# Optimization experiments

Measured on AMD Instinct MI355X. Metric: run time of the kernel, lower is better.

The kernel has to match this reference:

```python
import jax, jax.numpy as jnp
from jax import lax
import numpy as np

NS, NC = 12, 4            # n_state, n_ctrl
NSC = NS + NC             # tau = [x; u]
T, B = 50, 2048
U_LO, U_HI = -1.0, 1.0
LQR_ITERS = 3             # qp_iter-style outer LQR iterations
N_LS = 5                  # max_linesearch_iter
LS_DECAY = 0.5            # linesearch_decay


def setup_inputs() -> dict:
    key = jax.random.key(0)
    k0, k1, k2, k3, k4 = jax.random.split(key, 5)
    x0 = jax.random.normal(k0, (B, NS), jnp.float32)
    # PD quadratic cost: C = 0.1 * A A^T + I  (symmetric positive definite)
    A = jax.random.normal(k1, (T, B, NSC, NSC), jnp.float32) * (1.0 / np.sqrt(NSC))
    C = 0.1 * jnp.einsum('tbik,tbjk->tbij', A, A) + jnp.eye(NSC, dtype=jnp.float32)
    c = jax.random.normal(k2, (T, B, NSC), jnp.float32)
    # Near-identity stable linear dynamics x' = F [x;u] + f
    F = 0.02 * jax.random.normal(k3, (T, B, NS, NSC), jnp.float32)
    eye_pad = jnp.concatenate([0.98 * jnp.eye(NS, dtype=jnp.float32),
                               jnp.zeros((NS, NC), jnp.float32)], axis=-1)
    F = F + eye_pad
    f = 0.01 * jax.random.normal(k4, (T, B, NS), jnp.float32)
    return {'x0': x0, 'C': C, 'c': c, 'F': F, 'f': f}


def _riccati(C, c, F, f):
    """Backward Riccati recursion. Returns feedback gains K [T,B,NC,NS], k [T,B,NC]."""
    def step(carry, inp):
        V, v = carry                      # V: [B,NS,NS], v: [B,NS]
        Ct, ct, Ft, ft = inp
        FtV = jnp.einsum('bki,bkl->bil', Ft, V)          # F^T V: [B,NSC,NS]
        Q = Ct + jnp.einsum('bil,blj->bij', FtV, Ft)     # [B,NSC,NSC]
        q = ct + jnp.einsum('bki,bk->bi', Ft,
                            jnp.einsum('bij,bj->bi', V, ft) + v)
        Qxx, Qxu = Q[:, :NS, :NS], Q[:, :NS, NS:]
        Qux, Quu = Q[:, NS:, :NS], Q[:, NS:, NS:]
        qx, qu = q[:, :NS], q[:, NS:]
        rhs = jnp.concatenate([Qux, qu[:, :, None]], axis=-1)  # [B,NC,NS+1]
        sol = jnp.linalg.solve(Quu, rhs)
        K = -sol[:, :, :NS]               # [B,NC,NS]
        kk = -sol[:, :, NS]               # [B,NC]
        QxuK = jnp.einsum('bij,bjk->bik', Qxu, K)
        V_new = Qxx + QxuK + QxuK.transpose(0, 2, 1) \
            + jnp.einsum('bji,bjl,blk->bik', K, Quu, K)
        V_new = 0.5 * (V_new + V_new.transpose(0, 2, 1))
        v_new = qx + jnp.einsum('bij,bj->bi', Qxu, kk) \
            + jnp.einsum('bji,bj->bi', K, qu + jnp.einsum('bij,bj->bi', Quu, kk))
        return (V_new, v_new), (K, kk)

    Vz = jnp.zeros((C.shape[1], NS, NS), C.dtype)
    vz = jnp.zeros((C.shape[1], NS), C.dtype)
    _, (K, kk) = lax.scan(step, (Vz, vz), (C, c, F, f), reverse=True)
    return K, kk


def _rollout(alpha, x0, u_nom, K, kk, C, c, F, f):
    """Forward pass with box-clamped controls and line-search blending."""
    def step(carry, inp):
        x, cost = carry
        Ct, ct, Ft, ft, Kt, kt, unomt = inp
        u_lqr = jnp.einsum('bij,bj->bi', Kt, x) + kt
        u = jnp.clip((1.0 - alpha) * unomt + alpha * u_lqr, U_LO, U_HI)
        tau = jnp.concatenate([x, u], axis=-1)            # [B,NSC]
        cost = cost + 0.5 * jnp.einsum('bi,bij,bj->b', tau, Ct, tau) \
            + jnp.einsum('bi,bi->b', ct, tau)
        x_next = jnp.einsum('bij,bj->bi', Ft, tau) + ft
        return (x_next, cost), tau

    init = (x0, jnp.zeros(x0.shape[0], x0.dtype))
    (_, cost), taus = lax.scan(step, init, (C, c, F, f, K, kk, u_nom))
    return cost, taus  # cost [B], taus [T,B,NSC]


def reference(x0, C, c, F, f):
    alphas = LS_DECAY ** jnp.arange(N_LS, dtype=C.dtype)  # [N_LS]
    u_nom = jnp.zeros((T, x0.shape[0], NC), x0.dtype)
    taus = None
    for _ in range(LQR_ITERS):
        K, kk = _riccati(C, c, F, f)
        costs, taus_all = jax.vmap(
            lambda a: _rollout(a, x0, u_nom, K, kk, C, c, F, f))(alphas)
        # costs: [N_LS,B]; taus_all: [N_LS,T,B,NSC]. Pick best alpha per batch elem.
        best = jnp.argmin(costs, axis=0)                  # [B]
        taus = jnp.take_along_axis(taus_all,
                                   best[None, None, :, None], axis=0)[0]
        u_nom = taus[:, :, NS:]
    return taus  # [T, B, NSC] optimized trajectory [x; u]
```

## Files before the change

### kernel.cpp

```cpp
#include <hip/hip_runtime.h>
#include <math.h>

#define T_   50
#define B_   2048
#define NS_  12
#define NC_  4
#define NSC_ 16
#define LDC  20
#define TAUS_STRIDE 808

__device__ __forceinline__ float dot4f(const float4 a, const float4 b) {
    return a.x*b.x + a.y*b.y + a.z*b.z + a.w*b.w;
}
__device__ __forceinline__ void axpy4(float4& acc, float s, const float4 v) {
    acc.x += s*v.x; acc.y += s*v.y; acc.z += s*v.z; acc.w += s*v.w;
}

__device__ __forceinline__ void wsync() {
    __builtin_amdgcn_wave_barrier();
    __builtin_amdgcn_s_waitcnt(0xC07F);
    __builtin_amdgcn_wave_barrier();
}

__device__ __forceinline__ void bsync() {
    asm volatile("s_waitcnt lgkmcnt(0)\n\ts_barrier" ::: "memory");
}

struct RicPref { float4 rC, rAux; };

__device__ __forceinline__ RicPref ric_load(
    const float* Cg, const float* cg, const float* Fg, const float* fg,
    int t, int b, int lane)
{
    RicPref p;
    const size_t base = (size_t)t * B_ + b;
    p.rC = ((const float4*)(Cg + base*256))[lane];
    if (lane < 48)      p.rAux = ((const float4*)(Fg + base*192))[lane];
    else if (lane < 52) p.rAux = ((const float4*)(cg + base*16))[lane-48];
    else if (lane < 55) p.rAux = ((const float4*)(fg + base*12))[lane-52];
    return p;
}

__global__ __launch_bounds__(64) void riccati_kernel(
    const float* __restrict__ Cg, const float* __restrict__ cg,
    const float* __restrict__ Fg, const float* __restrict__ fg,
    float* __restrict__ Kk)
{
    const int b    = blockIdx.x;
    const int lane = threadIdx.x;

    __shared__ __align__(16) float sV[144];
    __shared__ __align__(16) float sv[12];
    __shared__ __align__(16) float sF[12*LDC];
    __shared__ __align__(16) float sC[16*LDC];
    __shared__ __align__(16) float sc[16];
    __shared__ __align__(16) float sf[12];
    __shared__ __align__(16) float sP[12*LDC];
    __shared__ __align__(16) float sQ[16*LDC];
    __shared__ __align__(16) float sq[16];
    __shared__ __align__(16) float stmp[12];
    __shared__ __align__(16) float sK[48];
    __shared__ __align__(16) float skk[4];
    __shared__ __align__(16) float sM[144];

    for (int i = lane; i < 144; i += 64) sV[i] = 0.f;
    if (lane < 12) sv[lane] = 0.f;

    RicPref cur = ric_load(Cg, cg, Fg, fg, T_-1, b, lane);
    wsync();

    for (int t = T_ - 1; t >= 0; --t) {
        const size_t base = (size_t)t * B_ + b;

        wsync();
        {
            const int row = lane >> 2, ch = (lane & 3) << 2;
            *(float4*)(sC + row*LDC + ch) = cur.rC;
            if (lane < 48)      *(float4*)(sF + row*LDC + ch) = cur.rAux;
            else if (lane < 52) ((float4*)sc)[lane-48] = cur.rAux;
            else if (lane < 55) ((float4*)sf)[lane-52] = cur.rAux;
        }
        RicPref nxt = ric_load(Cg, cg, Fg, fg, (t > 0) ? t-1 : 0, b, lane);
        wsync();

        if (lane < 48) {
            const int k = lane >> 2, jc = (lane & 3) << 2;
            float4 acc = make_float4(0.f,0.f,0.f,0.f);
            #pragma unroll
            for (int l = 0; l < 12; ++l) {
                axpy4(acc, sV[k*12 + l], *(const float4*)(sF + l*LDC + jc));
            }
            *(float4*)(sP + k*LDC + jc) = acc;
        } else if (lane < 60) {
            const int k = lane - 48;
            float acc = sv[k];
            #pragma unroll
            for (int l = 0; l < 12; ++l) acc += sV[k*12 + l] * sf[l];
            stmp[k] = acc;
        }
        wsync();

        {
            const int i = lane >> 2, jc = (lane & 3) << 2;
            float4 acc = *(const float4*)(sC + i*LDC + jc);
            #pragma unroll
            for (int k = 0; k < 12; ++k) {
                axpy4(acc, sF[k*LDC + i], *(const float4*)(sP + k*LDC + jc));
            }
            *(float4*)(sQ + i*LDC + jc) = acc;
        }
        if (lane < 16) {
            float acc = sc[lane];
            #pragma unroll
            for (int k = 0; k < 12; ++k) acc += sF[k*LDC + lane] * stmp[k];
            sq[lane] = acc;
        }
        wsync();

        {
            const float* Qu = sQ + 12*LDC + 12;
            const float a00=Qu[0],      a01=Qu[1],      a02=Qu[2],      a03=Qu[3];
            const float a11=Qu[LDC+1],  a12=Qu[LDC+2],  a13=Qu[LDC+3];
            const float a22=Qu[2*LDC+2],a23=Qu[2*LDC+3],a33=Qu[3*LDC+3];
            const float l00 = sqrtf(a00), i00 = 1.f/l00;
            const float l10 = a01*i00, l20 = a02*i00, l30 = a03*i00;
            const float l11 = sqrtf(a11 - l10*l10), i11 = 1.f/l11;
            const float l21 = (a12 - l20*l10)*i11;
            const float l31 = (a13 - l30*l10)*i11;
            const float l22 = sqrtf(a22 - l20*l20 - l21*l21), i22 = 1.f/l22;
            const float l32 = (a23 - l30*l20 - l31*l21)*i22;
            const float l33 = sqrtf(a33 - l30*l30 - l31*l31 - l32*l32), i33 = 1.f/l33;
            if (lane < 13) {
                float r0, r1, r2, r3;
                if (lane < 12) {
                    r0 = sQ[12*LDC + lane]; r1 = sQ[13*LDC + lane];
                    r2 = sQ[14*LDC + lane]; r3 = sQ[15*LDC + lane];
                } else {
                    r0 = sq[12]; r1 = sq[13]; r2 = sq[14]; r3 = sq[15];
                }
                const float y0 = r0*i00;
                const float y1 = (r1 - l10*y0)*i11;
                const float y2 = (r2 - l20*y0 - l21*y1)*i22;
                const float y3 = (r3 - l30*y0 - l31*y1 - l32*y2)*i33;
                const float z3 = y3*i33;
                const float z2 = (y2 - l32*z3)*i22;
                const float z1 = (y1 - l21*z2 - l31*z3)*i11;
                const float z0 = (y0 - l10*z1 - l20*z2 - l30*z3)*i00;
                if (lane < 12) {
                    sK[0*12+lane] = -z0; sK[1*12+lane] = -z1;
                    sK[2*12+lane] = -z2; sK[3*12+lane] = -z3;
                } else {
                    skk[0] = -z0; skk[1] = -z1; skk[2] = -z2; skk[3] = -z3;
                }
            }
        }
        wsync();

        if (lane < 52) {
            (Kk + base*52)[lane] = (lane < 48) ? sK[lane] : skk[lane-48];
        }
        if (lane < 36) {
            const int i = lane / 3, jc = (lane % 3) << 2;
            float4 acc = make_float4(0.f,0.f,0.f,0.f);
            #pragma unroll
            for (int m = 0; m < 4; ++m) {
                axpy4(acc, sK[m*12 + i], *(const float4*)(sQ + (12+m)*LDC + jc));
            }
            *(float4*)(sM + i*12 + jc) = acc;
        } else if (lane < 48) {
            const int i = lane - 36;
            float acc = sq[i];
            #pragma unroll
            for (int m = 0; m < 4; ++m) acc += sQ[i*LDC + 12 + m] * skk[m];
            sv[i] = acc;
        }
        wsync();

        if (lane < 36) {
            const int i = lane / 3, jc = (lane % 3) << 2;
            const float4 q  = *(const float4*)(sQ + i*LDC + jc);
            const float4 m1 = *(const float4*)(sM + i*12 + jc);
            const float t0 = sM[(jc+0)*12 + i];
            const float t1 = sM[(jc+1)*12 + i];
            const float t2 = sM[(jc+2)*12 + i];
            const float t3 = sM[(jc+3)*12 + i];
            float4 r;
            r.x = q.x + 0.5f*(m1.x + t0);
            r.y = q.y + 0.5f*(m1.y + t1);
            r.z = q.z + 0.5f*(m1.z + t2);
            r.w = q.w + 0.5f*(m1.w + t3);
            *(float4*)(sV + i*12 + jc) = r;
        }
        cur = nxt;
    }
}

struct RollAux { float4 r1, r2; };

__device__ __forceinline__ RollAux aux_load(
    const float* cg, const float* Fg, const float* fg, const float* Kk,
    int t, int b, int lane)
{
    RollAux p;
    const size_t base = (size_t)t * B_ + b;
    if (lane < 48)      p.r1 = ((const float4*)(Fg + base*192))[lane];
    else if (lane < 61) p.r1 = ((const float4*)(Kk + base*52))[lane-48];
    else                p.r1 = ((const float4*)(cg + base*16))[lane-61];
    if (lane == 0)      p.r2 = ((const float4*)(cg + base*16))[3];
    else if (lane < 4)  p.r2 = ((const float4*)(fg + base*12))[lane-1];
    return p;
}

__global__ __launch_bounds__(128, 4) void rollout_kernel(
    const float* __restrict__ x0g, const float* __restrict__ Cg,
    const float* __restrict__ cg,  const float* __restrict__ Fg,
    const float* __restrict__ fg,  const float* __restrict__ Kk,
    float* __restrict__ outg)
{
    const int b    = blockIdx.x;
    const int tid  = threadIdx.x;
    const int wave = tid >> 6;
    const int lane = tid & 63;

    __shared__ __align__(16) float staus[5*TAUS_STRIDE];
    __shared__ __align__(16) float sunom[T_*NC_];
    __shared__ __align__(16) float sx0[12];
    __shared__ __align__(16) float sC[16*LDC];
    __shared__ __align__(16) float sF[12*LDC];
    __shared__ __align__(16) float sKk[56];
    __shared__ __align__(16) float sc[16];
    __shared__ __align__(16) float sf[12];
    __shared__ float scost[5];
    __shared__ int   sbest;

    const int  task    = wave*64 + lane;
    const bool is_cost = task < 80;
    int a1, i1;
    if (is_cost) { a1 = task >> 4; i1 = task & 15; }
    else { const int v = task - 80; a1 = v / 12; i1 = v - a1*12; }
    const float* row1  = (is_cost ? (const float*)sC : (const float*)sF) + i1*LDC;
    const float* add1  = (is_cost ? (const float*)sc : (const float*)sf) + i1;
    float*       taub1 = staus + a1*TAUS_STRIDE;

    const int    iT    = (lane < 12) ? lane : 0;
    const float* rowT  = sF + iT*LDC;
    float*       taubT = staus + 4*TAUS_STRIDE;

    const int    aA  = (lane < 20) ? (lane >> 2) : 0;
    const int    iA  = lane & 3;
    const float  alA = ldexpf(1.0f, -aA);
    const float* KrA = sKk + iA*12;
    float*       tauA = staus + aA*TAUS_STRIDE;

    for (int i = tid; i < T_*NC_; i += 128) sunom[i] = 0.f;
    if (tid < 3) ((float4*)sx0)[tid] = ((const float4*)(x0g + (size_t)b*12))[tid];

    float4  curC;
    RollAux curA;
    if (wave == 0) curC = ((const float4*)(Cg + (size_t)b*256))[lane];
    else           curA = aux_load(cg, Fg, fg, Kk, 0, b, lane);
    bsync();

    for (int iter = 0; iter < 3; ++iter) {
        if (tid < 15) {
            const int a = tid / 3, ch = (tid % 3) << 2;
            *(float4*)(staus + a*TAUS_STRIDE + ch) = *(const float4*)(sx0 + ch);
        }
        float ca = 0.f;
        int toff = 0;

        for (int t = 0; t < T_; ++t) {
            bsync();
            if (wave == 0) {
                const int row = lane >> 2, ch = (lane & 3) << 2;
                *(float4*)(sC + row*LDC + ch) = curC;
                curC = ((const float4*)(Cg +
                          ((size_t)((t+1 < T_) ? t+1 : 0) * B_ + b)*256))[lane];
            } else {
                {
                    const int row = lane >> 2, ch = (lane & 3) << 2;
                    if (lane < 48)      *(float4*)(sF + row*LDC + ch) = curA.r1;
                    else if (lane < 61) ((float4*)sKk)[lane-48] = curA.r1;
                    else                ((float4*)sc)[lane-61]  = curA.r1;
                    if (lane == 0)      ((float4*)sc)[3] = curA.r2;
                    else if (lane < 4)  ((float4*)sf)[lane-1] = curA.r2;
                }
                curA = aux_load(cg, Fg, fg, Kk, (t+1 < T_) ? t+1 : 0, b, lane);
                wsync();
                if (lane < 20) {
                    const float* x = tauA + toff;
                    float ulqr = dot4f(*(const float4*)(KrA+0), *(const float4*)(x+0))
                               + dot4f(*(const float4*)(KrA+4), *(const float4*)(x+4))
                               + dot4f(*(const float4*)(KrA+8), *(const float4*)(x+8))
                               + sKk[48 + iA];
                    float u = (1.f - alA)*sunom[t*4 + iA] + alA*ulqr;
                    u = fminf(1.f, fmaxf(-1.f, u));
                    tauA[toff + 12 + iA] = u;
                }
            }
            bsync();

            const bool tnl = (t != T_-1);
            {
                const float* tau = taub1 + toff;
                const float  av  = add1[0];
                float acc = is_cost ? 0.f : av;
                acc += dot4f(*(const float4*)(row1+ 0), *(const float4*)(tau+ 0));
                acc += dot4f(*(const float4*)(row1+ 4), *(const float4*)(tau+ 4));
                acc += dot4f(*(const float4*)(row1+ 8), *(const float4*)(tau+ 8));
                acc += dot4f(*(const float4*)(row1+12), *(const float4*)(tau+12));
                if (is_cost)  ca += (0.5f*acc + av) * tau[i1];
                else if (tnl) taub1[toff + 16 + i1] = acc;
            }
            if (wave == 0 && lane < 12 && tnl) {
                const float* tau = taubT + toff;
                float acc = sf[iT];
                acc += dot4f(*(const float4*)(rowT+ 0), *(const float4*)(tau+ 0));
                acc += dot4f(*(const float4*)(rowT+ 4), *(const float4*)(tau+ 4));
                acc += dot4f(*(const float4*)(rowT+ 8), *(const float4*)(tau+ 8));
                acc += dot4f(*(const float4*)(rowT+12), *(const float4*)(tau+12));
                taubT[toff + 16 + iT] = acc;
            }
            toff += 16;
        }

        #pragma unroll
        for (int off = 1; off < 16; off <<= 1) ca += __shfl_xor(ca, off, 16);
        if (wave == 0) { if ((lane & 15) == 0) scost[lane >> 4] = ca; }
        else if (lane == 0) scost[4] = ca;
        bsync();
        if (tid == 0) {
            int bi = 0; float bc = scost[0];
            #pragma unroll
            for (int a = 1; a < 5; ++a) {
                if (scost[a] < bc) { bc = scost[a]; bi = a; }
            }
            sbest = bi;
        }
        bsync();
        const int best = sbest;

        for (int idx = tid; idx < T_*NC_; idx += 128) {
            const int tt = idx >> 2, i = idx & 3;
            sunom[idx] = staus[best*TAUS_STRIDE + tt*16 + 12 + i];
        }
        if (iter == 2) {
            for (int idx = tid; idx < T_*NSC_; idx += 128) {
                const int tt = idx >> 4, j = idx & 15;
                outg[((size_t)tt*B_ + b)*16 + j] = staus[best*TAUS_STRIDE + tt*16 + j];
            }
        }
        bsync();
    }
}

extern "C" void kernel_launch(void* const* d_in, const int* in_sizes, int n_in,
                              void* d_out, int out_size, void* d_ws, size_t ws_size,
                              hipStream_t stream) {
    const float* x0 = (const float*)d_in[0];
    const float* C  = (const float*)d_in[1];
    const float* c  = (const float*)d_in[2];
    const float* F  = (const float*)d_in[3];
    const float* f  = (const float*)d_in[4];
    float* out = (float*)d_out;
    float* Kk  = (float*)d_ws;

    riccati_kernel<<<B_, 64, 0, stream>>>(C, c, F, f, Kk);
    rollout_kernel<<<B_, 128, 0, stream>>>(x0, C, c, F, f, Kk, out);
}
```

Measured before the change: 444.2 us.

## Prefetch per-thread cost/dynamics rows into registers, drop shared staging

Each thread now loads from global memory, into registers, exactly the C/F row, the c/f scalar and the K row it needs for the next timestep, double-buffered across unrolled steps. This removes the shared-memory staging of C, F, K, c and f along with the extra wave sync. It also splits the dot products around the block barrier so the x-part is computed before u is known. The cost is more registers per thread and redundant or uncoalesced global loads, and occupancy could suffer under the launch bounds.

```diff
diff --git a/kernel.cpp b/kernel.cpp
--- a/kernel.cpp
+++ b/kernel.cpp
@@ -195,21 +195,7 @@
     }
 }
 
-struct RollAux { float4 r1, r2; };
-
-__device__ __forceinline__ RollAux aux_load(
-    const float* cg, const float* Fg, const float* fg, const float* Kk,
-    int t, int b, int lane)
-{
-    RollAux p;
-    const size_t base = (size_t)t * B_ + b;
-    if (lane < 48)      p.r1 = ((const float4*)(Fg + base*192))[lane];
-    else if (lane < 61) p.r1 = ((const float4*)(Kk + base*52))[lane-48];
-    else                p.r1 = ((const float4*)(cg + base*16))[lane-61];
-    if (lane == 0)      p.r2 = ((const float4*)(cg + base*16))[3];
-    else if (lane < 4)  p.r2 = ((const float4*)(fg + base*12))[lane-1];
-    return p;
-}
+struct RollPref { float4 row[4]; float4 aux[4]; float s0, s1; };
 
 __global__ __launch_bounds__(128, 4) void rollout_kernel(
     const float* __restrict__ x0g, const float* __restrict__ Cg,
@@ -225,11 +211,6 @@
     __shared__ __align__(16) float staus[5*TAUS_STRIDE];
     __shared__ __align__(16) float sunom[T_*NC_];
     __shared__ __align__(16) float sx0[12];
-    __shared__ __align__(16) float sC[16*LDC];
-    __shared__ __align__(16) float sF[12*LDC];
-    __shared__ __align__(16) float sKk[56];
-    __shared__ __align__(16) float sc[16];
-    __shared__ __align__(16) float sf[12];
     __shared__ float scost[5];
     __shared__ int   sbest;
 
@@ -238,27 +219,98 @@
     int a1, i1;
     if (is_cost) { a1 = task >> 4; i1 = task & 15; }
     else { const int v = task - 80; a1 = v / 12; i1 = v - a1*12; }
-    const float* row1  = (is_cost ? (const float*)sC : (const float*)sF) + i1*LDC;
-    const float* add1  = (is_cost ? (const float*)sc : (const float*)sf) + i1;
-    float*       taub1 = staus + a1*TAUS_STRIDE;
-
-    const int    iT    = (lane < 12) ? lane : 0;
-    const float* rowT  = sF + iT*LDC;
-    float*       taubT = staus + 4*TAUS_STRIDE;
-
-    const int    aA  = (lane < 20) ? (lane >> 2) : 0;
-    const int    iA  = lane & 3;
-    const float  alA = ldexpf(1.0f, -aA);
-    const float* KrA = sKk + iA*12;
-    float*       tauA = staus + aA*TAUS_STRIDE;
+    float* taub1 = staus + a1*TAUS_STRIDE;
+
+    const int iT = (lane < 12) ? lane : 11;
+    float* taubT = staus + 4*TAUS_STRIDE;
+
+    const int   aA  = (lane < 20) ? (lane >> 2) : 0;
+    const int   iA  = lane & 3;
+    const float alA = ldexpf(1.0f, -aA);
+
+    const float *rowB, *auxB, *s0B, *s1B;
+    int rowS, auxS, s0S, s1S;
+    if (wave == 0) {
+        rowB = Cg + (size_t)b*256 + i1*16;  rowS = B_*256;
+        s0B  = cg + (size_t)b*16  + i1;     s0S  = B_*16;
+        auxB = Fg + (size_t)b*192 + iT*16;  auxS = B_*192;
+        s1B  = fg + (size_t)b*12  + iT;     s1S  = B_*12;
+    } else {
+        if (is_cost) { rowB = Cg + (size_t)b*256 + i1*16; rowS = B_*256;
+                       s0B  = cg + (size_t)b*16  + i1;    s0S  = B_*16; }
+        else         { rowB = Fg + (size_t)b*192 + i1*16; rowS = B_*192;
+                       s0B  = fg + (size_t)b*12  + i1;    s0S  = B_*12; }
+        auxB = Kk + (size_t)b*52 + iA*12;   auxS = B_*52;
+        s1B  = Kk + (size_t)b*52 + 48 + iA; s1S  = B_*52;
+    }
+
+    auto load_pref = [&](RollPref& p, int tn) {
+        const float* rp = rowB + tn*rowS;
+        p.row[0] = *(const float4*)(rp);
+        p.row[1] = *(const float4*)(rp + 4);
+        p.row[2] = *(const float4*)(rp + 8);
+        p.row[3] = *(const float4*)(rp + 12);
+        const float* ap = auxB + tn*auxS;
+        p.aux[0] = *(const float4*)(ap);
+        p.aux[1] = *(const float4*)(ap + 4);
+        p.aux[2] = *(const float4*)(ap + 8);
+        p.aux[3] = *(const float4*)(ap + 12);
+        p.s0 = *(s0B + tn*s0S);
+        p.s1 = *(s1B + tn*s1S);
+    };
+
+    auto do_step = [&](RollPref& cur, RollPref& nxt, int t, int toff, float& ca) {
+        bsync();
+        const int tn = (t+1 < T_) ? t+1 : 0;
+        load_pref(nxt, tn);
+
+        if (wave == 1 && lane < 20) {
+            const float* xp = staus + aA*TAUS_STRIDE + toff;
+            float ulqr = dot4f(cur.aux[0], *(const float4*)(xp))
+                       + dot4f(cur.aux[1], *(const float4*)(xp+4))
+                       + dot4f(cur.aux[2], *(const float4*)(xp+8))
+                       + cur.s1;
+            float u = (1.f - alA)*sunom[t*4 + iA] + alA*ulqr;
+            u = fminf(1.f, fmaxf(-1.f, u));
+            staus[aA*TAUS_STRIDE + toff + 12 + iA] = u;
+        }
+
+        const float* tp = taub1 + toff;
+        float acc = is_cost ? 0.f : cur.s0;
+        acc += dot4f(cur.row[0], *(const float4*)(tp));
+        acc += dot4f(cur.row[1], *(const float4*)(tp+4));
+        acc += dot4f(cur.row[2], *(const float4*)(tp+8));
+
+        float accT = 0.f;
+        if (wave == 0 && lane < 12) {
+            const float* tq = taubT + toff;
+            accT = cur.s1;
+            accT += dot4f(cur.aux[0], *(const float4*)(tq));
+            accT += dot4f(cur.aux[1], *(const float4*)(tq+4));
+            accT += dot4f(cur.aux[2], *(const float4*)(tq+8));
+        }
+
+        bsync();
+
+        acc += dot4f(cur.row[3], *(const float4*)(taub1 + toff + 12));
+        const bool tnl = (t != T_-1);
+        if (is_cost) {
+            const float ti = taub1[toff + i1];
+            ca += (0.5f*acc + cur.s0) * ti;
+        } else if (tnl) {
+            taub1[toff + 16 + i1] = acc;
+        }
+        if (wave == 0 && lane < 12 && tnl) {
+            accT += dot4f(cur.aux[3], *(const float4*)(taubT + toff + 12));
+            taubT[toff + 16 + iT] = accT;
+        }
+    };
 
     for (int i = tid; i < T_*NC_; i += 128) sunom[i] = 0.f;
     if (tid < 3) ((float4*)sx0)[tid] = ((const float4*)(x0g + (size_t)b*12))[tid];
 
-    float4  curC;
-    RollAux curA;
-    if (wave == 0) curC = ((const float4*)(Cg + (size_t)b*256))[lane];
-    else           curA = aux_load(cg, Fg, fg, Kk, 0, b, lane);
+    RollPref R0, R1;
+    load_pref(R0, 0);
     bsync();
 
     for (int iter = 0; iter < 3; ++iter) {
@@ -267,61 +319,10 @@
             *(float4*)(staus + a*TAUS_STRIDE + ch) = *(const float4*)(sx0 + ch);
         }
         float ca = 0.f;
-        int toff = 0;
-
-        for (int t = 0; t < T_; ++t) {
-            bsync();
-            if (wave == 0) {
-                const int row = lane >> 2, ch = (lane & 3) << 2;
-                *(float4*)(sC + row*LDC + ch) = curC;
-                curC = ((const float4*)(Cg +
-                          ((size_t)((t+1 < T_) ? t+1 : 0) * B_ + b)*256))[lane];
-            } else {
-                {
-                    const int row = lane >> 2, ch = (lane & 3) << 2;
-                    if (lane < 48)      *(float4*)(sF + row*LDC + ch) = curA.r1;
-                    else if (lane < 61) ((float4*)sKk)[lane-48] = curA.r1;
-                    else                ((float4*)sc)[lane-61]  = curA.r1;
-                    if (lane == 0)      ((float4*)sc)[3] = curA.r2;
-                    else if (lane < 4)  ((float4*)sf)[lane-1] = curA.r2;
-                }
-                curA = aux_load(cg, Fg, fg, Kk, (t+1 < T_) ? t+1 : 0, b, lane);
-                wsync();
-                if (lane < 20) {
-                    const float* x = tauA + toff;
-                    float ulqr = dot4f(*(const float4*)(KrA+0), *(const float4*)(x+0))
-                               + dot4f(*(const float4*)(KrA+4), *(const float4*)(x+4))
-                               + dot4f(*(const float4*)(KrA+8), *(const float4*)(x+8))
-                               + sKk[48 + iA];
-                    float u = (1.f - alA)*sunom[t*4 + iA] + alA*ulqr;
-                    u = fminf(1.f, fmaxf(-1.f, u));
-                    tauA[toff + 12 + iA] = u;
-                }
-            }
-            bsync();
-
-            const bool tnl = (t != T_-1);
-            {
-                const float* tau = taub1 + toff;
-                const float  av  = add1[0];
-                float acc = is_cost ? 0.f : av;
-                acc += dot4f(*(const float4*)(row1+ 0), *(const float4*)(tau+ 0));
-                acc += dot4f(*(const float4*)(row1+ 4), *(const float4*)(tau+ 4));
-                acc += dot4f(*(const float4*)(row1+ 8), *(const float4*)(tau+ 8));
-                acc += dot4f(*(const float4*)(row1+12), *(const float4*)(tau+12));
-                if (is_cost)  ca += (0.5f*acc + av) * tau[i1];
-                else if (tnl) taub1[toff + 16 + i1] = acc;
-            }
-            if (wave == 0 && lane < 12 && tnl) {
-                const float* tau = taubT + toff;
-                float acc = sf[iT];
-                acc += dot4f(*(const float4*)(rowT+ 0), *(const float4*)(tau+ 0));
-                acc += dot4f(*(const float4*)(rowT+ 4), *(const float4*)(tau+ 4));
-                acc += dot4f(*(const float4*)(rowT+ 8), *(const float4*)(tau+ 8));
-                acc += dot4f(*(const float4*)(rowT+12), *(const float4*)(tau+12));
-                taubT[toff + 16 + iT] = acc;
-            }
-            toff += 16;
+
+        for (int t = 0; t < T_; t += 2) {
+            do_step(R0, R1, t,   t*16,     ca);
+            do_step(R1, R0, t+1, t*16+16,  ca);
         }
 
         #pragma unroll
```

Result: slower. 632.9 us (+42.5%).
